# Kernel optimization log

Measured on AMD Instinct MI355X. Metric: run time of the kernel, lower is better.

Reference implementation:

```python
import jax, jax.numpy as jnp
import numpy as np

HIDDEN = 512
B, N = 32, 96

def setup_inputs() -> dict:
    key = jax.random.key(0)
    k1, k2, k3, k4, k5 = jax.random.split(key, 5)
    h = HIDDEN
    s1 = 1.0 / np.sqrt(2 * h)
    s2 = 1.0 / np.sqrt(h)
    return {
        "encoded_sequence": jax.random.normal(k1, (B, N, h), dtype=jnp.float32),
        "W1": jax.random.uniform(k2, (h, 2 * h), dtype=jnp.float32, minval=-s1, maxval=s1),
        "b1": jax.random.uniform(k3, (h,), dtype=jnp.float32, minval=-s1, maxval=s1),
        "W2": jax.random.uniform(k4, (1, h), dtype=jnp.float32, minval=-s2, maxval=s2),
        "b2": jax.random.uniform(k5, (1,), dtype=jnp.float32, minval=-s2, maxval=s2),
    }

def reference(encoded_sequence, W1, b1, W2, b2):
    # Faithful to calc_arc_scores: arc_vectors[b,i,j] = concat(X[b,i], X[b,j]),
    # scores = Linear2(tanh(Linear1(arc_vectors))).squeeze(-1).
    # Fused (biaffine) form: split W1 into head/dep halves and broadcast-sum,
    # avoiding the O(B*n^2*2h) concatenated intermediate.
    h = W1.shape[0]
    X = encoded_sequence
    Wa = W1[:, :h]   # acts on X_i (first half of concat)
    Wb = W1[:, h:]   # acts on X_j (second half of concat)
    Ha = jnp.einsum('bnh,kh->bnk', X, Wa)            # [B, n, h]
    Hb = jnp.einsum('bnh,kh->bnk', X, Wb)            # [B, n, h]
    T = jnp.tanh(Ha[:, :, None, :] + Hb[:, None, :, :] + b1)  # [B, n, n, h]
    arc_scores = jnp.einsum('bijk,k->bij', T, W2[0]) + b2[0]   # [B, n, n]
    return arc_scores
```

## Files before the change

### kernel.cpp

```cpp
#include <hip/hip_runtime.h>
#include <hip/hip_bf16.h>

#define NN 96
#define C_TANH 2.8853900817779268f

typedef __attribute__((ext_vector_type(4))) float    f32x4;
typedef __attribute__((ext_vector_type(2))) float    f32x2;
typedef __attribute__((ext_vector_type(8))) short    short8;
typedef __attribute__((ext_vector_type(8))) _Float16 half8;

static __device__ inline unsigned int cvt_pk_bf16(float lo, float hi) {
    unsigned int r;
    asm("v_cvt_pk_bf16_f32 %0, %1, %2" : "=v"(r) : "v"(lo), "v"(hi));
    return r;
}

__global__ __launch_bounds__(256) void gemm_h(const float* __restrict__ X,
                                              const float* __restrict__ W1,
                                              const float* __restrict__ b1,
                                              _Float16* __restrict__ Ea,
                                              _Float16* __restrict__ Eh) {
    __shared__ unsigned short As[2][2048];
    __shared__ unsigned short Bs[2][2048];

    int bid  = blockIdx.x;
    int xcd  = bid & 7;
    int sub  = bid >> 3;
    int mloc = sub % 6;
    int nq   = sub / 6;
    int mb   = (xcd * 6 + mloc) * 64;
    int nb   = nq * 64;
    int tid = threadIdx.x;
    int w   = tid >> 6;
    int l   = tid & 63;

    int srow = tid >> 2;
    int sg   = (tid & 3) * 8;
    int scs  = sg ^ ((srow & 3) << 3);
    const float* asrc = X + (mb + srow) * 512 + sg;
    int nrow = nb + srow;
    const float* bsrc = W1 + (nrow & 511) * 1024 + ((nrow >> 9) << 9) + sg;
    unsigned short* adst = &As[0][srow * 32 + scs];
    unsigned short* bdst = &Bs[0][srow * 32 + scs];

    struct Regs { f32x4 a0, a1, b0, b4; };
    Regs RA, RB;

#define LOADR(R, k0)                                                          \
    {                                                                         \
        R.a0 = *(const f32x4*)(asrc + (k0));                                  \
        R.a1 = *(const f32x4*)(asrc + (k0) + 4);                              \
        R.b0 = *(const f32x4*)(bsrc + (k0));                                  \
        R.b4 = *(const f32x4*)(bsrc + (k0) + 4);                              \
    }
#define WRITER(R, buf)                                                        \
    {                                                                         \
        uint4 ua, ub;                                                         \
        ua.x = cvt_pk_bf16(R.a0[0], R.a0[1]); ua.y = cvt_pk_bf16(R.a0[2], R.a0[3]); \
        ua.z = cvt_pk_bf16(R.a1[0], R.a1[1]); ua.w = cvt_pk_bf16(R.a1[2], R.a1[3]); \
        ub.x = cvt_pk_bf16(R.b0[0], R.b0[1]); ub.y = cvt_pk_bf16(R.b0[2], R.b0[3]); \
        ub.z = cvt_pk_bf16(R.b4[0], R.b4[1]); ub.w = cvt_pk_bf16(R.b4[2], R.b4[3]); \
        *(uint4*)(adst + (buf) * 2048) = ua;                                  \
        *(uint4*)(bdst + (buf) * 2048) = ub;                                  \
    }

    int lr    = l & 15;
    int koffs = ((l >> 4) * 8) ^ ((lr & 3) << 3);
    int aoff  = (16 * w + lr) * 32 + koffs;
    int boff0 = lr * 32 + koffs;

    f32x4 acc[4] = {};

#define COMPUTE(cur)                                                          \
    {                                                                         \
        short8 afr = *(const short8*)(&As[cur][aoff]);                        \
        short8 bfr[4];                                                        \
        _Pragma("unroll")                                                     \
        for (int t = 0; t < 4; ++t)                                           \
            bfr[t] = *(const short8*)(&Bs[cur][boff0 + t * 512]);             \
        _Pragma("unroll")                                                     \
        for (int t = 0; t < 4; ++t)                                           \
            acc[t] = __builtin_amdgcn_mfma_f32_16x16x32_bf16(afr, bfr[t],     \
                                                             acc[t], 0, 0, 0);\
    }

    LOADR(RA, 0)
    WRITER(RA, 0)
    LOADR(RB, 32)
    __syncthreads();
#pragma unroll 1
    for (int kk = 0; kk < 7; ++kk) {
        LOADR(RA, (2 * kk + 2) * 32)
        COMPUTE(0)
        WRITER(RB, 1)
        __syncthreads();
        LOADR(RB, (2 * kk + 3) * 32)
        COMPUTE(1)
        WRITER(RA, 0)
        __syncthreads();
    }
    COMPUTE(0)
    WRITER(RB, 1)
    __syncthreads();
    COMPUTE(1)
#undef LOADR
#undef WRITER
#undef COMPUTE

    int r0 = (l >> 4) * 4;
    bool isB = (nb >= 512);
    int colbase = nb & 511;
    _Float16* dst = isB ? Eh : Ea;
#pragma unroll
    for (int t = 0; t < 4; ++t) {
        int col = colbase + 16 * t + lr;
        float bias = isB ? b1[col] : 0.0f;
#pragma unroll
        for (int q = 0; q < 4; ++q) {
            int m = mb + 16 * w + r0 + q;
            float arg = (acc[t][q] + bias) * C_TANH;
            dst[m * 512 + col] = (_Float16)exp2f(arg);
        }
    }
}

__global__ __launch_bounds__(256) void arc_kernel(const _Float16* __restrict__ Ea,
                                                  const _Float16* __restrict__ Eh,
                                                  const float* __restrict__ w2,
                                                  const float* __restrict__ b2,
                                                  float* __restrict__ out) {
    __shared__ _Float16 a_s[16 * 512];
    __shared__ _Float16 h_s[16 * 512];
    __shared__ float    red[3][64][4];

    int bid = blockIdx.x;
    int xcd = bid & 7;
    int sub = bid >> 3;
    int b   = xcd * 4 + sub / 36;
    int r   = sub % 36;
    int it  = r / 6;
    int jt  = r % 6;
    int tid = threadIdx.x;

    const _Float16* asrc = Ea + (b * NN + it * 16) * 512;
    const _Float16* hsrc = Eh + (b * NN + jt * 16) * 512;

#pragma unroll
    for (int p = 0; p < 4; ++p) {
        int idx = tid + p * 256;
        int row = idx >> 6, c = idx & 63;
        int cs = c ^ (row & 7);
        *(f32x4*)(a_s + row * 512 + cs * 8) = *(const f32x4*)(asrc + row * 512 + c * 8);
        *(f32x4*)(h_s + row * 512 + cs * 8) = *(const f32x4*)(hsrc + row * 512 + c * 8);
    }
    __syncthreads();

    int w  = tid >> 6;
    int kq = __builtin_amdgcn_readfirstlane(w);
    int l  = tid & 63;
    int pi = l >> 3;
    int pj = l & 7;
    int r0a = pi * 2, r1a = r0a + 1;
    int r0h = pj * 2, r1h = r0h + 1;

    const _Float16* a0 = a_s + r0a * 512 + kq * 128;
    const _Float16* a1 = a_s + r1a * 512 + kq * 128;
    const _Float16* h0 = h_s + r0h * 512 + kq * 128;
    const _Float16* h1 = h_s + r1h * 512 + kq * 128;
    int sa0 = r0a & 7, sa1 = r1a & 7, sh0 = r0h & 7, sh1 = r1h & 7;
    const float* wp = w2 + kq * 128;

    float acc00 = 0.f, acc01 = 0.f, acc10 = 0.f, acc11 = 0.f;

#define PROC(av, hv, acc)                                                     \
    {                                                                         \
        float s0 = __builtin_fmaf((float)av[0], (float)hv[0], 1.0f);          \
        float s1 = __builtin_fmaf((float)av[1], (float)hv[1], 1.0f);          \
        float s2 = __builtin_fmaf((float)av[2], (float)hv[2], 1.0f);          \
        float s3 = __builtin_fmaf((float)av[3], (float)hv[3], 1.0f);          \
        float s4 = __builtin_fmaf((float)av[4], (float)hv[4], 1.0f);          \
        float s5 = __builtin_fmaf((float)av[5], (float)hv[5], 1.0f);          \
        float s6 = __builtin_fmaf((float)av[6], (float)hv[6], 1.0f);          \
        float s7 = __builtin_fmaf((float)av[7], (float)hv[7], 1.0f);          \
        float n0 = __builtin_fmaf(wv1, s0, wv0 * s1);                         \
        float n1 = __builtin_fmaf(wv3, s2, wv2 * s3);                         \
        float n2 = __builtin_fmaf(wv5, s4, wv4 * s5);                         \
        float n3 = __builtin_fmaf(wv7, s6, wv6 * s7);                         \
        acc = __builtin_fmaf(n0, __builtin_amdgcn_rcpf(s0 * s1), acc);        \
        acc = __builtin_fmaf(n1, __builtin_amdgcn_rcpf(s2 * s3), acc);        \
        acc = __builtin_fmaf(n2, __builtin_amdgcn_rcpf(s4 * s5), acc);        \
        acc = __builtin_fmaf(n3, __builtin_amdgcn_rcpf(s6 * s7), acc);        \
    }

#pragma unroll 4
    for (int c = 0; c < 16; ++c) {
        half8 av0 = *(const half8*)(a0 + ((c ^ sa0) << 3));
        half8 av1 = *(const half8*)(a1 + ((c ^ sa1) << 3));
        half8 hv0 = *(const half8*)(h0 + ((c ^ sh0) << 3));
        half8 hv1 = *(const half8*)(h1 + ((c ^ sh1) << 3));
        f32x4 wlo = *(const f32x4*)(wp + c * 8);
        f32x4 whi = *(const f32x4*)(wp + c * 8 + 4);
        float wv0 = wlo[0], wv1 = wlo[1], wv2 = wlo[2], wv3 = wlo[3];
        float wv4 = whi[0], wv5 = whi[1], wv6 = whi[2], wv7 = whi[3];
        PROC(av0, hv0, acc00)
        PROC(av0, hv1, acc01)
        PROC(av1, hv0, acc10)
        PROC(av1, hv1, acc11)
    }
#undef PROC

    if (w != 0) {
        f32x4 v = {acc00, acc01, acc10, acc11};
        *(f32x4*)(&red[w - 1][l][0]) = v;
    }
    __syncthreads();

    if (w == 0) {
#pragma unroll
        for (int rr = 0; rr < 3; ++rr) {
            f32x4 v = *(const f32x4*)(&red[rr][l][0]);
            acc00 += v[0]; acc01 += v[1]; acc10 += v[2]; acc11 += v[3];
        }
        f32x4 v0 = *(const f32x4*)(w2 + l * 8);
        f32x4 v1 = *(const f32x4*)(w2 + l * 8 + 4);
        float sv = (v0[0] + v0[1]) + (v0[2] + v0[3])
                 + (v1[0] + v1[1]) + (v1[2] + v1[3]);
#pragma unroll
        for (int off = 32; off; off >>= 1) sv += __shfl_xor(sv, off, 64);
        float Sv = sv + b2[0];

        int i0 = it * 16 + r0a;
        int j0 = jt * 16 + r0h;
        f32x2 o0 = {__builtin_fmaf(-2.f, acc00, Sv), __builtin_fmaf(-2.f, acc01, Sv)};
        f32x2 o1 = {__builtin_fmaf(-2.f, acc10, Sv), __builtin_fmaf(-2.f, acc11, Sv)};
        *(f32x2*)(out + (b * NN + i0) * NN + j0)     = o0;
        *(f32x2*)(out + (b * NN + i0 + 1) * NN + j0) = o1;
    }
}

extern "C" void kernel_launch(void* const* d_in, const int* in_sizes, int n_in,
                              void* d_out, int out_size, void* d_ws, size_t ws_size,
                              hipStream_t stream) {
    (void)in_sizes; (void)n_in; (void)out_size; (void)ws_size;

    const float* X  = (const float*)d_in[0];
    const float* W1 = (const float*)d_in[1];
    const float* b1 = (const float*)d_in[2];
    const float* W2 = (const float*)d_in[3];
    const float* b2 = (const float*)d_in[4];
    float* out = (float*)d_out;

    char* ws = (char*)d_ws;
    _Float16* Ea = (_Float16*)(ws);
    _Float16* Eh = (_Float16*)(ws + 3145728);

    gemm_h<<<768, 256, 0, stream>>>(X, W1, b1, Ea, Eh);
    arc_kernel<<<1152, 256, 0, stream>>>(Ea, Eh, W2, b2, out);
}
```

Before: 35.83 us.

## Drop LDS staging in arc kernel; use 4x4 register tiles with shuffle-reduced K

The arc kernel no longer stages the Ea/Eh tiles in shared memory. Each lane now loads half8 chunks straight from global memory and computes a 4x4 block of (i,j) outputs in registers, which raises per-lane reuse of loaded data. The K dimension is split across four lane groups inside each wave plus four waves, and partial sums are combined with xor-shuffles and a smaller LDS reduction. This removes the LDS fill and its barrier, but the 16 accumulators and 8 vector loads per step raise register pressure, and the global loads now depend on L1/L2 hit rates.

```diff
diff --git a/kernel.cpp b/kernel.cpp
--- a/kernel.cpp
+++ b/kernel.cpp
@@ -129,9 +129,7 @@
                                                   const float* __restrict__ w2,
                                                   const float* __restrict__ b2,
                                                   float* __restrict__ out) {
-    __shared__ _Float16 a_s[16 * 512];
-    __shared__ _Float16 h_s[16 * 512];
-    __shared__ float    red[3][64][4];
+    __shared__ float red[3][16][16];
 
     int bid = blockIdx.x;
     int xcd = bid & 7;
@@ -141,36 +139,19 @@
     int it  = r / 6;
     int jt  = r % 6;
     int tid = threadIdx.x;
-
-    const _Float16* asrc = Ea + (b * NN + it * 16) * 512;
-    const _Float16* hsrc = Eh + (b * NN + jt * 16) * 512;
-
-#pragma unroll
-    for (int p = 0; p < 4; ++p) {
-        int idx = tid + p * 256;
-        int row = idx >> 6, c = idx & 63;
-        int cs = c ^ (row & 7);
-        *(f32x4*)(a_s + row * 512 + cs * 8) = *(const f32x4*)(asrc + row * 512 + c * 8);
-        *(f32x4*)(h_s + row * 512 + cs * 8) = *(const f32x4*)(hsrc + row * 512 + c * 8);
-    }
-    __syncthreads();
-
-    int w  = tid >> 6;
-    int kq = __builtin_amdgcn_readfirstlane(w);
-    int l  = tid & 63;
-    int pi = l >> 3;
-    int pj = l & 7;
-    int r0a = pi * 2, r1a = r0a + 1;
-    int r0h = pj * 2, r1h = r0h + 1;
-
-    const _Float16* a0 = a_s + r0a * 512 + kq * 128;
-    const _Float16* a1 = a_s + r1a * 512 + kq * 128;
-    const _Float16* h0 = h_s + r0h * 512 + kq * 128;
-    const _Float16* h1 = h_s + r1h * 512 + kq * 128;
-    int sa0 = r0a & 7, sa1 = r1a & 7, sh0 = r0h & 7, sh1 = r1h & 7;
-    const float* wp = w2 + kq * 128;
-
-    float acc00 = 0.f, acc01 = 0.f, acc10 = 0.f, acc11 = 0.f;
+    int w   = tid >> 6;
+    int kq  = __builtin_amdgcn_readfirstlane(w);
+    int l   = tid & 63;
+    int pos = l & 15;
+    int ip  = pos >> 2;
+    int jp  = pos & 3;
+    int ksub = l >> 4;
+
+    const _Float16* abase = Ea + (b * NN + it * 16 + ip * 4) * 512 + kq * 128 + ksub * 8;
+    const _Float16* hbase = Eh + (b * NN + jt * 16 + jp * 4) * 512 + kq * 128 + ksub * 8;
+    const float*    wp    = w2 + kq * 128 + ksub * 8;
+
+    float acc[4][4] = {};
 
 #define PROC(av, hv, acc)                                                     \
     {                                                                         \
@@ -192,35 +173,45 @@
         acc = __builtin_fmaf(n3, __builtin_amdgcn_rcpf(s6 * s7), acc);        \
     }
 
-#pragma unroll 4
-    for (int c = 0; c < 16; ++c) {
-        half8 av0 = *(const half8*)(a0 + ((c ^ sa0) << 3));
-        half8 av1 = *(const half8*)(a1 + ((c ^ sa1) << 3));
-        half8 hv0 = *(const half8*)(h0 + ((c ^ sh0) << 3));
-        half8 hv1 = *(const half8*)(h1 + ((c ^ sh1) << 3));
-        f32x4 wlo = *(const f32x4*)(wp + c * 8);
-        f32x4 whi = *(const f32x4*)(wp + c * 8 + 4);
+#pragma unroll
+    for (int itr = 0; itr < 4; ++itr) {
+        int ko = itr * 32;
+        half8 av[4], hv[4];
+#pragma unroll
+        for (int rr = 0; rr < 4; ++rr) {
+            av[rr] = *(const half8*)(abase + rr * 512 + ko);
+            hv[rr] = *(const half8*)(hbase + rr * 512 + ko);
+        }
+        f32x4 wlo = *(const f32x4*)(wp + ko);
+        f32x4 whi = *(const f32x4*)(wp + ko + 4);
         float wv0 = wlo[0], wv1 = wlo[1], wv2 = wlo[2], wv3 = wlo[3];
         float wv4 = whi[0], wv5 = whi[1], wv6 = whi[2], wv7 = whi[3];
-        PROC(av0, hv0, acc00)
-        PROC(av0, hv1, acc01)
-        PROC(av1, hv0, acc10)
-        PROC(av1, hv1, acc11)
+#pragma unroll
+        for (int rr = 0; rr < 4; ++rr)
+#pragma unroll
+            for (int cc = 0; cc < 4; ++cc)
+                PROC(av[rr], hv[cc], acc[rr][cc])
     }
 #undef PROC
 
-    if (w != 0) {
-        f32x4 v = {acc00, acc01, acc10, acc11};
-        *(f32x4*)(&red[w - 1][l][0]) = v;
+#pragma unroll
+    for (int rr = 0; rr < 4; ++rr)
+#pragma unroll
+        for (int cc = 0; cc < 4; ++cc) {
+            acc[rr][cc] += __shfl_xor(acc[rr][cc], 16, 64);
+            acc[rr][cc] += __shfl_xor(acc[rr][cc], 32, 64);
+        }
+
+    if (w != 0 && l < 16) {
+#pragma unroll
+        for (int rr = 0; rr < 4; ++rr) {
+            f32x4 v = {acc[rr][0], acc[rr][1], acc[rr][2], acc[rr][3]};
+            *(f32x4*)(&red[w - 1][pos][rr * 4]) = v;
+        }
     }
     __syncthreads();
 
     if (w == 0) {
-#pragma unroll
-        for (int rr = 0; rr < 3; ++rr) {
-            f32x4 v = *(const f32x4*)(&red[rr][l][0]);
-            acc00 += v[0]; acc01 += v[1]; acc10 += v[2]; acc11 += v[3];
-        }
         f32x4 v0 = *(const f32x4*)(w2 + l * 8);
         f32x4 v1 = *(const f32x4*)(w2 + l * 8 + 4);
         float sv = (v0[0] + v0[1]) + (v0[2] + v0[3])
@@ -229,12 +220,23 @@
         for (int off = 32; off; off >>= 1) sv += __shfl_xor(sv, off, 64);
         float Sv = sv + b2[0];
 
-        int i0 = it * 16 + r0a;
-        int j0 = jt * 16 + r0h;
-        f32x2 o0 = {__builtin_fmaf(-2.f, acc00, Sv), __builtin_fmaf(-2.f, acc01, Sv)};
-        f32x2 o1 = {__builtin_fmaf(-2.f, acc10, Sv), __builtin_fmaf(-2.f, acc11, Sv)};
-        *(f32x2*)(out + (b * NN + i0) * NN + j0)     = o0;
-        *(f32x2*)(out + (b * NN + i0 + 1) * NN + j0) = o1;
+        if (l < 16) {
+#pragma unroll
+            for (int rr = 0; rr < 4; ++rr) {
+                f32x4 p0 = *(const f32x4*)(&red[0][pos][rr * 4]);
+                f32x4 p1 = *(const f32x4*)(&red[1][pos][rr * 4]);
+                f32x4 p2 = *(const f32x4*)(&red[2][pos][rr * 4]);
+                f32x4 o;
+#pragma unroll
+                for (int cc = 0; cc < 4; ++cc) {
+                    float a = acc[rr][cc] + p0[cc] + p1[cc] + p2[cc];
+                    o[cc] = __builtin_fmaf(-2.f, a, Sv);
+                }
+                int i = it * 16 + ip * 4 + rr;
+                int j = jt * 16 + jp * 4;
+                *(f32x4*)(out + (b * NN + i) * NN + j) = o;
+            }
+        }
     }
 }
 
```

Measured after the change: 44.76 us. 1.25x slower.

## Enlarge gemm_h tiles to 128x128 with 512-thread blocks and 2x4 warp fragments

Applied to the files above, without the earlier changes.

The projection GEMM now uses 128x128 output tiles per block with 8 waves arranged 4x2. Each wave computes a 32x64 sub-tile with 2x4 MFMA fragments, which reuses the A and B fragments loaded from LDS. The grid shrinks from 768 to 192 blocks. This is meant to cut global and LDS traffic per output, but it lowers the block count on a GPU with many CUs and doubles shared memory per block.

```diff
diff --git a/kernel.cpp b/kernel.cpp
--- a/kernel.cpp
+++ b/kernel.cpp
@@ -15,21 +15,21 @@
     return r;
 }
 
-__global__ __launch_bounds__(256) void gemm_h(const float* __restrict__ X,
-                                              const float* __restrict__ W1,
-                                              const float* __restrict__ b1,
-                                              _Float16* __restrict__ Ea,
-                                              _Float16* __restrict__ Eh) {
-    __shared__ unsigned short As[2][2048];
-    __shared__ unsigned short Bs[2][2048];
+__global__ __launch_bounds__(512, 2) void gemm_h(const float* __restrict__ X,
+                                                 const float* __restrict__ W1,
+                                                 const float* __restrict__ b1,
+                                                 _Float16* __restrict__ Ea,
+                                                 _Float16* __restrict__ Eh) {
+    __shared__ unsigned short As[2][4096];
+    __shared__ unsigned short Bs[2][4096];
 
     int bid  = blockIdx.x;
     int xcd  = bid & 7;
     int sub  = bid >> 3;
-    int mloc = sub % 6;
-    int nq   = sub / 6;
-    int mb   = (xcd * 6 + mloc) * 64;
-    int nb   = nq * 64;
+    int mloc = sub % 3;
+    int nq   = sub / 3;
+    int mb   = (xcd * 3 + mloc) * 128;
+    int nb   = nq * 128;
     int tid = threadIdx.x;
     int w   = tid >> 6;
     int l   = tid & 63;
@@ -60,28 +60,34 @@
         ua.z = cvt_pk_bf16(R.a1[0], R.a1[1]); ua.w = cvt_pk_bf16(R.a1[2], R.a1[3]); \
         ub.x = cvt_pk_bf16(R.b0[0], R.b0[1]); ub.y = cvt_pk_bf16(R.b0[2], R.b0[3]); \
         ub.z = cvt_pk_bf16(R.b4[0], R.b4[1]); ub.w = cvt_pk_bf16(R.b4[2], R.b4[3]); \
-        *(uint4*)(adst + (buf) * 2048) = ua;                                  \
-        *(uint4*)(bdst + (buf) * 2048) = ub;                                  \
+        *(uint4*)(adst + (buf) * 4096) = ua;                                  \
+        *(uint4*)(bdst + (buf) * 4096) = ub;                                  \
     }
 
     int lr    = l & 15;
     int koffs = ((l >> 4) * 8) ^ ((lr & 3) << 3);
-    int aoff  = (16 * w + lr) * 32 + koffs;
-    int boff0 = lr * 32 + koffs;
-
-    f32x4 acc[4] = {};
+    int wm    = w >> 1;
+    int wn    = w & 1;
+    int aoff0 = (32 * wm + lr) * 32 + koffs;
+    int boff0 = (64 * wn + lr) * 32 + koffs;
+
+    f32x4 acc[2][4] = {};
 
 #define COMPUTE(cur)                                                          \
     {                                                                         \
-        short8 afr = *(const short8*)(&As[cur][aoff]);                        \
-        short8 bfr[4];                                                        \
+        short8 afr[2], bfr[4];                                                \
+        _Pragma("unroll")                                                     \
+        for (int mf = 0; mf < 2; ++mf)                                        \
+            afr[mf] = *(const short8*)(&As[cur][aoff0 + mf * 512]);           \
         _Pragma("unroll")                                                     \
         for (int t = 0; t < 4; ++t)                                           \
             bfr[t] = *(const short8*)(&Bs[cur][boff0 + t * 512]);             \
         _Pragma("unroll")                                                     \
-        for (int t = 0; t < 4; ++t)                                           \
-            acc[t] = __builtin_amdgcn_mfma_f32_16x16x32_bf16(afr, bfr[t],     \
-                                                             acc[t], 0, 0, 0);\
+        for (int mf = 0; mf < 2; ++mf)                                        \
+            _Pragma("unroll")                                                 \
+            for (int t = 0; t < 4; ++t)                                       \
+                acc[mf][t] = __builtin_amdgcn_mfma_f32_16x16x32_bf16(         \
+                    afr[mf], bfr[t], acc[mf][t], 0, 0, 0);                    \
     }
 
     LOADR(RA, 0)
@@ -113,14 +119,16 @@
     _Float16* dst = isB ? Eh : Ea;
 #pragma unroll
     for (int t = 0; t < 4; ++t) {
-        int col = colbase + 16 * t + lr;
+        int col = colbase + 64 * wn + 16 * t + lr;
         float bias = isB ? b1[col] : 0.0f;
 #pragma unroll
-        for (int q = 0; q < 4; ++q) {
-            int m = mb + 16 * w + r0 + q;
-            float arg = (acc[t][q] + bias) * C_TANH;
-            dst[m * 512 + col] = (_Float16)exp2f(arg);
-        }
+        for (int mf = 0; mf < 2; ++mf)
+#pragma unroll
+            for (int q = 0; q < 4; ++q) {
+                int m = mb + 32 * wm + 16 * mf + r0 + q;
+                float arg = (acc[mf][t][q] + bias) * C_TANH;
+                dst[m * 512 + col] = (_Float16)exp2f(arg);
+            }
     }
 }
 
@@ -254,6 +262,6 @@
     _Float16* Ea = (_Float16*)(ws);
     _Float16* Eh = (_Float16*)(ws + 3145728);
 
-    gemm_h<<<768, 256, 0, stream>>>(X, W1, b1, Ea, Eh);
+    gemm_h<<<192, 512, 0, stream>>>(X, W1, b1, Ea, Eh);
     arc_kernel<<<1152, 256, 0, stream>>>(Ea, Eh, W2, b2, out);
 }
```

Measured after the change: 35.17 us. No clear change (-1.8%).

## Fuse projection GEMM and arc scoring into one cooperative persistent kernel

Applied to the files above, without the earlier changes.

Replaces the two-launch pipeline (projection GEMM, then arc-score kernel) with a single cooperative kernel of 256 blocks of 512 threads. The GEMM phase writes exp-transformed projections, a grid-wide sync follows, and the same blocks then compute the arc scores with new tilings (96x128 GEMM tiles, 24x24 score tiles with a cross-wave reduction in LDS). This removes one kernel launch and the gap between the two kernels, at the cost of a grid barrier, fewer blocks and lower parallelism in each phase. If the cooperative launch fails, it falls back to the old two kernels.

```diff
diff --git a/kernel.cpp b/kernel.cpp
--- a/kernel.cpp
+++ b/kernel.cpp
@@ -1,5 +1,8 @@
 #include <hip/hip_runtime.h>
 #include <hip/hip_bf16.h>
+#include <hip/hip_cooperative_groups.h>
+
+namespace cg = cooperative_groups;
 
 #define NN 96
 #define C_TANH 2.8853900817779268f
@@ -13,6 +16,271 @@
     unsigned int r;
     asm("v_cvt_pk_bf16_f32 %0, %1, %2" : "=v"(r) : "v"(lo), "v"(hi));
     return r;
+}
+
+__global__ __launch_bounds__(512, 2) void fused_kernel(
+        const float* __restrict__ X, const float* __restrict__ W1,
+        const float* __restrict__ b1, const float* __restrict__ w2,
+        const float* __restrict__ b2, _Float16* __restrict__ Ea,
+        _Float16* __restrict__ Eh, float* __restrict__ out) {
+    __shared__ __align__(16) char smem[65280];
+
+    int bid = blockIdx.x;
+    int tid = threadIdx.x;
+    int xcd = bid & 7;
+    int sub = bid >> 3;
+    int w   = tid >> 6;
+    int l   = tid & 63;
+
+    {
+        unsigned short* lds = (unsigned short*)smem;
+        int mloc = sub & 3;
+        int nq   = sub >> 2;
+        int mb   = xcd * 384 + mloc * 96;
+        int nb   = nq * 128;
+
+        const float* csrc0;
+        const float* csrc1 = X;
+        int cdst0, cdst1 = 0;
+        if (tid < 384) {
+            int ar = tid >> 2, g = tid & 3;
+            csrc0 = X + (mb + ar) * 512 + g * 8;
+            cdst0 = ar * 32 + ((g * 8) ^ ((ar & 3) << 3));
+            int br = (128 + tid) >> 2, g2 = tid & 3;
+            int nrow = nb + br;
+            csrc1 = W1 + (nrow & 511) * 1024 + ((nrow >> 9) << 9) + g2 * 8;
+            cdst1 = (96 + br) * 32 + ((g2 * 8) ^ ((br & 3) << 3));
+        } else {
+            int br = (tid - 384) >> 2, g = (tid - 384) & 3;
+            int nrow = nb + br;
+            csrc0 = W1 + (nrow & 511) * 1024 + ((nrow >> 9) << 9) + g * 8;
+            cdst0 = (96 + br) * 32 + ((g * 8) ^ ((br & 3) << 3));
+        }
+
+        struct R2 { f32x4 a0, a1, b0, b1; };
+        R2 RA, RB;
+
+#define LOADR(R, k0)                                                          \
+        {                                                                     \
+            R.a0 = *(const f32x4*)(csrc0 + (k0));                             \
+            R.a1 = *(const f32x4*)(csrc0 + (k0) + 4);                         \
+            if (tid < 384) {                                                  \
+                R.b0 = *(const f32x4*)(csrc1 + (k0));                         \
+                R.b1 = *(const f32x4*)(csrc1 + (k0) + 4);                     \
+            }                                                                 \
+        }
+#define WRITER(R, buf)                                                        \
+        {                                                                     \
+            uint4 u;                                                          \
+            u.x = cvt_pk_bf16(R.a0[0], R.a0[1]); u.y = cvt_pk_bf16(R.a0[2], R.a0[3]); \
+            u.z = cvt_pk_bf16(R.a1[0], R.a1[1]); u.w = cvt_pk_bf16(R.a1[2], R.a1[3]); \
+            *(uint4*)(lds + (buf) * 7168 + cdst0) = u;                        \
+            if (tid < 384) {                                                  \
+                uint4 v;                                                      \
+                v.x = cvt_pk_bf16(R.b0[0], R.b0[1]); v.y = cvt_pk_bf16(R.b0[2], R.b0[3]); \
+                v.z = cvt_pk_bf16(R.b1[0], R.b1[1]); v.w = cvt_pk_bf16(R.b1[2], R.b1[3]); \
+                *(uint4*)(lds + (buf) * 7168 + cdst1) = v;                    \
+            }                                                                 \
+        }
+
+        int lr    = l & 15;
+        int koffs = ((l >> 4) * 8) ^ ((lr & 3) << 3);
+        int boff  = (96 + 16 * w + lr) * 32 + koffs;
+
+        f32x4 acc[6] = {};
+
+#define COMPUTE(cur)                                                          \
+        {                                                                     \
+            const unsigned short* base = lds + (cur) * 7168;                  \
+            short8 bfr = *(const short8*)(base + boff);                       \
+            _Pragma("unroll")                                                 \
+            for (int rf = 0; rf < 6; ++rf) {                                  \
+                short8 afr = *(const short8*)(base + (16 * rf + lr) * 32 + koffs); \
+                acc[rf] = __builtin_amdgcn_mfma_f32_16x16x32_bf16(afr, bfr,   \
+                                                              acc[rf], 0, 0, 0); \
+            }                                                                 \
+        }
+
+        LOADR(RA, 0)
+        WRITER(RA, 0)
+        LOADR(RB, 32)
+        __syncthreads();
+#pragma unroll 1
+        for (int kk = 0; kk < 7; ++kk) {
+            LOADR(RA, (2 * kk + 2) * 32)
+            COMPUTE(0)
+            WRITER(RB, 1)
+            __syncthreads();
+            LOADR(RB, (2 * kk + 3) * 32)
+            COMPUTE(1)
+            WRITER(RA, 0)
+            __syncthreads();
+        }
+        COMPUTE(0)
+        WRITER(RB, 1)
+        __syncthreads();
+        COMPUTE(1)
+#undef LOADR
+#undef WRITER
+#undef COMPUTE
+
+        int r0 = (l >> 4) * 4;
+        bool isB = (nb >= 512);
+        int col  = (nb & 511) + 16 * w + lr;
+        float bias = isB ? b1[col] : 0.0f;
+        _Float16* dst = isB ? Eh : Ea;
+#pragma unroll
+        for (int rf = 0; rf < 6; ++rf)
+#pragma unroll
+            for (int q = 0; q < 4; ++q) {
+                int m = mb + 16 * rf + r0 + q;
+                float arg = (acc[rf][q] + bias) * C_TANH;
+                dst[m * 512 + col] = (_Float16)exp2f(arg);
+            }
+    }
+
+    __threadfence();
+    cg::this_grid().sync();
+
+    {
+        _Float16* a_s = (_Float16*)smem;
+        _Float16* h_s = (_Float16*)(smem + 24576);
+        float*    red = (float*)(smem + 49152);
+
+        int bloc = sub >> 3;
+        int rem  = sub & 7;
+        int it   = rem >> 1;
+        int jp   = rem & 1;
+        int b    = xcd * 4 + bloc;
+
+        const _Float16* asrc = Ea + (b * NN + it * 24) * 512;
+#pragma unroll
+        for (int p = 0; p < 3; ++p) {
+            int idx = tid + p * 512;
+            int row = idx >> 6, c = idx & 63, cs = c ^ (row & 7);
+            *(f32x4*)(a_s + row * 512 + cs * 8) =
+                *(const f32x4*)(asrc + row * 512 + c * 8);
+        }
+
+        int kq = __builtin_amdgcn_readfirstlane(w);
+        int pi = l >> 3;
+        int pj = l & 7;
+        const float* wp = w2 + kq * 64;
+        float Sv = 0.f;
+
+        const _Float16* pa[3];
+        int sa[3];
+#pragma unroll
+        for (int d = 0; d < 3; ++d) {
+            int ra = 3 * pi + d;
+            pa[d] = a_s + ra * 512 + kq * 64;
+            sa[d] = ra & 7;
+        }
+
+#define FPROC(av, hv, acc)                                                    \
+        {                                                                     \
+            float s0 = __builtin_fmaf((float)av[0], (float)hv[0], 1.0f);      \
+            float s1 = __builtin_fmaf((float)av[1], (float)hv[1], 1.0f);      \
+            float s2 = __builtin_fmaf((float)av[2], (float)hv[2], 1.0f);      \
+            float s3 = __builtin_fmaf((float)av[3], (float)hv[3], 1.0f);      \
+            float s4 = __builtin_fmaf((float)av[4], (float)hv[4], 1.0f);      \
+            float s5 = __builtin_fmaf((float)av[5], (float)hv[5], 1.0f);      \
+            float s6 = __builtin_fmaf((float)av[6], (float)hv[6], 1.0f);      \
+            float s7 = __builtin_fmaf((float)av[7], (float)hv[7], 1.0f);      \
+            float n0 = __builtin_fmaf(wv1, s0, wv0 * s1);                     \
+            float n1 = __builtin_fmaf(wv3, s2, wv2 * s3);                     \
+            float n2 = __builtin_fmaf(wv5, s4, wv4 * s5);                     \
+            float n3 = __builtin_fmaf(wv7, s6, wv6 * s7);                     \
+            acc = __builtin_fmaf(n0, __builtin_amdgcn_rcpf(s0 * s1), acc);    \
+            acc = __builtin_fmaf(n1, __builtin_amdgcn_rcpf(s2 * s3), acc);    \
+            acc = __builtin_fmaf(n2, __builtin_amdgcn_rcpf(s4 * s5), acc);    \
+            acc = __builtin_fmaf(n3, __builtin_amdgcn_rcpf(s6 * s7), acc);    \
+        }
+
+#pragma unroll 1
+        for (int jj = 0; jj < 2; ++jj) {
+            int jt = jp * 2 + jj;
+            const _Float16* hsrc = Eh + (b * NN + jt * 24) * 512;
+#pragma unroll
+            for (int p = 0; p < 3; ++p) {
+                int idx = tid + p * 512;
+                int row = idx >> 6, c = idx & 63, cs = c ^ (row & 7);
+                *(f32x4*)(h_s + row * 512 + cs * 8) =
+                    *(const f32x4*)(hsrc + row * 512 + c * 8);
+            }
+            __syncthreads();
+
+            float acc[3][3] = {};
+            const _Float16* ph[3];
+            int sh[3];
+#pragma unroll
+            for (int d = 0; d < 3; ++d) {
+                int rh = 3 * pj + d;
+                ph[d] = h_s + rh * 512 + kq * 64;
+                sh[d] = rh & 7;
+            }
+
+#pragma unroll
+            for (int c = 0; c < 8; ++c) {
+                half8 av[3], hv[3];
+#pragma unroll
+                for (int d = 0; d < 3; ++d) {
+                    av[d] = *(const half8*)(pa[d] + ((c ^ sa[d]) << 3));
+                    hv[d] = *(const half8*)(ph[d] + ((c ^ sh[d]) << 3));
+                }
+                f32x4 wlo = *(const f32x4*)(wp + c * 8);
+                f32x4 whi = *(const f32x4*)(wp + c * 8 + 4);
+                float wv0 = wlo[0], wv1 = wlo[1], wv2 = wlo[2], wv3 = wlo[3];
+                float wv4 = whi[0], wv5 = whi[1], wv6 = whi[2], wv7 = whi[3];
+#pragma unroll
+                for (int di = 0; di < 3; ++di)
+#pragma unroll
+                    for (int dj = 0; dj < 3; ++dj)
+                        FPROC(av[di], hv[dj], acc[di][dj])
+            }
+
+            if (w != 0) {
+                float* rp = red + ((w - 1) * 64 + l) * 9;
+#pragma unroll
+                for (int di = 0; di < 3; ++di)
+#pragma unroll
+                    for (int dj = 0; dj < 3; ++dj)
+                        rp[di * 3 + dj] = acc[di][dj];
+            }
+            __syncthreads();
+
+            if (w == 0) {
+#pragma unroll
+                for (int rr = 0; rr < 7; ++rr) {
+                    const float* rp = red + (rr * 64 + l) * 9;
+#pragma unroll
+                    for (int di = 0; di < 3; ++di)
+#pragma unroll
+                        for (int dj = 0; dj < 3; ++dj)
+                            acc[di][dj] += rp[di * 3 + dj];
+                }
+                if (jj == 0) {
+                    f32x4 v0 = *(const f32x4*)(w2 + l * 8);
+                    f32x4 v1 = *(const f32x4*)(w2 + l * 8 + 4);
+                    float sv = (v0[0] + v0[1]) + (v0[2] + v0[3])
+                             + (v1[0] + v1[1]) + (v1[2] + v1[3]);
+#pragma unroll
+                    for (int off = 32; off; off >>= 1) sv += __shfl_xor(sv, off, 64);
+                    Sv = sv + b2[0];
+                }
+#pragma unroll
+                for (int di = 0; di < 3; ++di) {
+                    int i = it * 24 + 3 * pi + di;
+                    float* op = out + (b * NN + i) * NN + jt * 24 + 3 * pj;
+#pragma unroll
+                    for (int dj = 0; dj < 3; ++dj)
+                        op[dj] = __builtin_fmaf(-2.f, acc[di][dj], Sv);
+                }
+            }
+            __syncthreads();
+        }
+#undef FPROC
+    }
 }
 
 __global__ __launch_bounds__(256) void gemm_h(const float* __restrict__ X,
@@ -254,6 +522,13 @@
     _Float16* Ea = (_Float16*)(ws);
     _Float16* Eh = (_Float16*)(ws + 3145728);
 
-    gemm_h<<<768, 256, 0, stream>>>(X, W1, b1, Ea, Eh);
-    arc_kernel<<<1152, 256, 0, stream>>>(Ea, Eh, W2, b2, out);
+    void* args[8] = {(void*)&X, (void*)&W1, (void*)&b1, (void*)&W2,
+                     (void*)&b2, (void*)&Ea, (void*)&Eh, (void*)&out};
+    hipError_t e = hipLaunchCooperativeKernel(fused_kernel, dim3(256), dim3(512),
+                                              args, 0u, stream);
+    if (e != hipSuccess) {
+        (void)hipGetLastError();
+        gemm_h<<<768, 256, 0, stream>>>(X, W1, b1, Ea, Eh);
+        arc_kernel<<<1152, 256, 0, stream>>>(Ea, Eh, W2, b2, out);
+    }
 }
```

Result: slower. 125.0 us (+248.8%).
